# Performance work log

Measured on AMD Instinct MI355X. Metric: run time of the kernel, lower is better.

The kernel has to match this reference:

```python
import jax, jax.numpy as jnp
import numpy as np

R = 10000   # relation_num
E = 256     # emb_size == hidden_size
B = 1024    # batch
L = 8       # body length (loop runs L-1 steps)


def setup_inputs() -> dict:
    key = jax.random.key(0)
    ks = jax.random.split(key, 10)
    s = 0.05
    return {
        "bodys": jax.random.randint(ks[0], (B, L), 0, R),
        "emb_w": jax.random.normal(ks[1], (R, E), jnp.float32) * s,
        "w_ih": jax.random.normal(ks[2], (4 * E, E), jnp.float32) * s,
        "w_hh": jax.random.normal(ks[3], (4 * E, E), jnp.float32) * s,
        "b_ih": jax.random.normal(ks[4], (4 * E,), jnp.float32) * s,
        "b_hh": jax.random.normal(ks[5], (4 * E,), jnp.float32) * s,
        "fc1_w": jax.random.normal(ks[6], (E, 2 * E), jnp.float32) * s,
        "fc1_b": jax.random.normal(ks[7], (E,), jnp.float32) * s,
        "fc2_w": jax.random.normal(ks[8], (R + 1, E), jnp.float32) * s,
        "fc2_b": jax.random.normal(ks[9], (R + 1,), jnp.float32) * s,
    }


def _lstm(x, w_ih, w_hh, b_ih, b_hh):
    # x: [B, L, E] -> hidden states [B, L, H] (torch gate order i,f,g,o)
    Bn, _, H = x.shape[0], x.shape[1], w_hh.shape[1]
    h0 = jnp.zeros((Bn, H), x.dtype)
    c0 = jnp.zeros((Bn, H), x.dtype)

    def step(carry, xt):
        h, c = carry
        g = xt @ w_ih.T + b_ih + h @ w_hh.T + b_hh
        i, f, gg, o = jnp.split(g, 4, axis=-1)
        c = jax.nn.sigmoid(f) * c + jax.nn.sigmoid(i) * jnp.tanh(gg)
        h = jax.nn.sigmoid(o) * jnp.tanh(c)
        return (h, c), h

    _, hs = jax.lax.scan(step, (h0, c0), x.transpose(1, 0, 2))
    return hs.transpose(1, 0, 2)


def reference(bodys, emb_w, w_ih, w_hh, b_ih, b_hh, fc1_w, fc1_b, fc2_w, fc2_b):
    x = emb_w[bodys]                       # [B, L, E] embedded body relations
    body_hid = _lstm(x, w_ih, w_hh, b_ih, b_hh)  # [B, L, E]
    Rn = emb_w.shape[0]
    prob = emb_concat = prob_sf = None
    for i in range(body_hid.shape[1] - 1):   # short fixed unroll (L-1 steps)
        if i == 0:
            emb_1 = x[:, 0, :]
            second = x[:, 1, :]
        else:
            # prob_sf @ cat(embedding(indices), body_hid[:, i])  without [B,R+1,E]
            emb_1 = prob_sf[:, :Rn] @ emb_w + prob_sf[:, Rn:] * body_hid[:, i, :]
            # relation_emb[:, i+1, :] == emb_w[i+1] broadcast over batch
            second = jnp.broadcast_to(emb_w[i + 1], emb_1.shape)
        emb_concat = jnp.concatenate([emb_1, second], axis=1)   # [B, 2E]
        prob = jax.nn.relu(emb_concat @ fc1_w.T + fc1_b) @ fc2_w.T + fc2_b  # [B, R+1]
        prob_sf = jax.nn.softmax(prob, axis=1)
    return prob, emb_concat
```

## Files before the change

### kernel.cpp

```cpp
#include <hip/hip_runtime.h>

#define Bv 1024
#define Ev 256
#define Lv 8
#define Rv 10000
#define NP1 10001
#define PS2 10240
#define NPAD 10112
#define BM 64
#define BN 128
#define NSLICE 16
#define NSLOT 158
#define RPSTRIDE 160

typedef __attribute__((ext_vector_type(8))) short bf16x8;
typedef __attribute__((ext_vector_type(4))) float f32x4;

__device__ __forceinline__ float b2f(unsigned short u) {
    union { unsigned int i; float f; } v; v.i = ((unsigned int)u) << 16; return v.f;
}
__device__ __forceinline__ unsigned short f2b(float f) {
    union { float f; unsigned int i; } v; v.f = f;
    unsigned int r = v.i + 0x7fffu + ((v.i >> 16) & 1u);
    return (unsigned short)(r >> 16);
}
__device__ __forceinline__ void glds16(const void* g, void* l) {
    __builtin_amdgcn_global_load_lds(
        (const __attribute__((address_space(1))) void*)g,
        (__attribute__((address_space(3))) void*)l, 16, 0, 0);
}

__global__ __launch_bounds__(256) void gemm_tile(
    const unsigned short* __restrict__ A1, int lda1,
    const unsigned short* __restrict__ W1, int ldw1,
    const float* __restrict__ bias1,
    int Ktot, int kchunk, int Ncols, int mode,
    float* __restrict__ outF, unsigned short* __restrict__ outB, int ldc,
    float* __restrict__ rowPart, float* __restrict__ sfLastU)
{
    __shared__ unsigned short As[2][BM * 32];
    __shared__ unsigned short Bs[2][BN * 32];

    int bmode = mode & 7;
    int swz   = mode >> 4;
    int bx, by, bz;
    if (swz == 1) {
        int r = blockIdx.x & 7, q = blockIdx.x >> 3;
        bx = q & 15; by = r + (q >> 4) * 8; bz = 0;
        if (by >= NPAD / BN) return;
    } else if (swz == 2) {
        int r = blockIdx.x & 7, q = blockIdx.x >> 3;
        bz = r + (q >> 5) * 8; bx = (q & 31) >> 1; by = q & 1;
    } else {
        bx = blockIdx.x; by = blockIdx.y; bz = blockIdx.z;
    }

    int tid  = threadIdx.x;
    int wave = tid >> 6;
    int lane = tid & 63;
    int quad = lane >> 4;
    int l16  = lane & 15;
    int wm = (wave & 1) * 32;
    int wn = (wave >> 1) * 64;
    int m0 = bx * BM;
    int n0 = by * BN;
    int k0 = bz * kchunk;
    int k1 = k0 + kchunk; if (k1 > Ktot) k1 = Ktot;

    f32x4 acc[2][4];
#pragma unroll
    for (int i = 0; i < 2; ++i)
#pragma unroll
        for (int j = 0; j < 4; ++j) acc[i][j] = (f32x4){0.f, 0.f, 0.f, 0.f};

    int c0 = tid, c1 = 256 + tid;
    int row0 = c0 >> 2, row1 = c1 >> 2;
    int g80 = ((c0 & 3) ^ (row0 & 3) ^ ((row0 >> 2) & 3)) * 8;
    int g81 = ((c1 & 3) ^ (row1 & 3) ^ ((row1 >> 2) & 3)) * 8;

    bool first = true;
    for (int k = k0; k < k1; k += 64) {
        if (!first) __syncthreads();
        first = false;
#pragma unroll
        for (int h = 0; h < 2; ++h) {
            int kk = k + h * 32;
            glds16(A1 + (size_t)(m0 + row0) * lda1 + kk + g80, As[h] + (wave * 64) * 8);
            glds16(W1 + (size_t)(n0 + row0) * ldw1 + kk + g80, Bs[h] + (wave * 64) * 8);
            glds16(W1 + (size_t)(n0 + row1) * ldw1 + kk + g81, Bs[h] + (256 + wave * 64) * 8);
        }
        asm volatile("s_waitcnt vmcnt(0)" ::: "memory");
        __syncthreads();

#pragma unroll
        for (int h = 0; h < 2; ++h) {
            bf16x8 af[2], bfr[4];
#pragma unroll
            for (int t = 0; t < 2; ++t) {
                int m = wm + t * 16 + l16;
                int ca = quad ^ (m & 3) ^ ((m >> 2) & 3);
                af[t] = *(const bf16x8*)(As[h] + m * 32 + ca * 8);
            }
#pragma unroll
            for (int t = 0; t < 4; ++t) {
                int n = wn + t * 16 + l16;
                int cb = quad ^ (n & 3) ^ ((n >> 2) & 3);
                bfr[t] = *(const bf16x8*)(Bs[h] + n * 32 + cb * 8);
            }
#pragma unroll
            for (int i = 0; i < 2; ++i)
#pragma unroll
                for (int j = 0; j < 4; ++j)
                    acc[i][j] = __builtin_amdgcn_mfma_f32_16x16x32_bf16(
                        af[i], bfr[j], acc[i][j], 0, 0, 0);
        }
    }

    if (bmode == 5) {
        float rsum[2][4];
#pragma unroll
        for (int i = 0; i < 2; ++i)
#pragma unroll
            for (int r = 0; r < 4; ++r) rsum[i][r] = 0.f;
#pragma unroll
        for (int j = 0; j < 4; ++j) {
            int n = n0 + wn + j * 16 + l16;
            bool valid = (n < Ncols);
            float bsum = valid ? bias1[n] : 0.f;
#pragma unroll
            for (int i = 0; i < 2; ++i) {
                int mBase = m0 + wm + i * 16 + quad * 4;
#pragma unroll
                for (int r = 0; r < 4; ++r) {
                    float e = 0.f;
                    unsigned short w = 0;
                    if (valid) {
                        e = expf(acc[i][j][r] + bsum);
                        w = f2b(e);
                        if (n == Rv) sfLastU[mBase + r] = e;
                    }
                    outB[(size_t)(mBase + r) * ldc + n] = w;
                    rsum[i][r] += e;
                }
            }
        }
        int slot = by * 2 + (wn >> 6);
#pragma unroll
        for (int i = 0; i < 2; ++i)
#pragma unroll
            for (int r = 0; r < 4; ++r) {
                float s = rsum[i][r];
                s += __shfl_xor(s, 1);
                s += __shfl_xor(s, 2);
                s += __shfl_xor(s, 4);
                s += __shfl_xor(s, 8);
                if (l16 == 0) {
                    int m = m0 + wm + i * 16 + quad * 4 + r;
                    rowPart[(size_t)m * RPSTRIDE + slot] = s;
                }
            }
        return;
    }

#pragma unroll
    for (int j = 0; j < 4; ++j) {
        int n = n0 + wn + j * 16 + l16;
        bool valid = (n < Ncols);
        if (!valid && bmode != 3) continue;
        float bsum = (valid && bias1) ? bias1[n] : 0.f;
#pragma unroll
        for (int i = 0; i < 2; ++i) {
            int mBase = m0 + wm + i * 16 + quad * 4;
#pragma unroll
            for (int r = 0; r < 4; ++r) {
                float v = acc[i][j][r] + bsum;
                size_t idx = (size_t)(mBase + r) * ldc + n;
                if (bmode == 0)      outF[idx] = v;
                else if (bmode == 3) outB[idx] = valid ? f2b(v) : (unsigned short)0;
                else                 outB[(size_t)bz * (Bv * Ev) + idx] = f2b(v);
            }
        }
    }
}

__global__ __launch_bounds__(256) void gemm64(
    const unsigned short* __restrict__ A1, int lda1,
    const unsigned short* __restrict__ W1, int ldw1,
    const float* __restrict__ bias1,
    int Ktot, int Ncols, int mode,
    float* __restrict__ outF, unsigned short* __restrict__ outB,
    int ldc, int nshift,
    const float* __restrict__ xgate, int tstep)
{
    __shared__ unsigned short As[2][64 * 32];
    __shared__ unsigned short Bs[2][64 * 32];

    int bmode = mode & 7;
    int bx = blockIdx.x >> nshift;
    int by = blockIdx.x & ((1 << nshift) - 1);
    int tid  = threadIdx.x;
    int wave = tid >> 6;
    int lane = tid & 63;
    int quad = lane >> 4;
    int l16  = lane & 15;
    int m0 = bx * 64;
    int n0 = by * 64;

    f32x4 acc[4];
#pragma unroll
    for (int j = 0; j < 4; ++j) acc[j] = (f32x4){0.f, 0.f, 0.f, 0.f};

    int row = tid >> 2;
    int g8  = ((tid & 3) ^ (row & 3) ^ ((row >> 2) & 3)) * 8;

    bool first = true;
    for (int k = 0; k < Ktot; k += 64) {
        if (!first) __syncthreads();
        first = false;
#pragma unroll
        for (int h = 0; h < 2; ++h) {
            int kk = k + h * 32;
            glds16(A1 + (size_t)(m0 + row) * lda1 + kk + g8, As[h] + wave * 512);
            glds16(W1 + (size_t)(n0 + row) * ldw1 + kk + g8, Bs[h] + wave * 512);
        }
        asm volatile("s_waitcnt vmcnt(0)" ::: "memory");
        __syncthreads();

#pragma unroll
        for (int h = 0; h < 2; ++h) {
            int ml = wave * 16 + l16;
            int ca = quad ^ (ml & 3) ^ ((ml >> 2) & 3);
            bf16x8 a = *(const bf16x8*)(As[h] + ml * 32 + ca * 8);
#pragma unroll
            for (int j = 0; j < 4; ++j) {
                int nl = j * 16 + l16;
                int cb = quad ^ (nl & 3) ^ ((nl >> 2) & 3);
                bf16x8 b = *(const bf16x8*)(Bs[h] + nl * 32 + cb * 8);
                acc[j] = __builtin_amdgcn_mfma_f32_16x16x32_bf16(a, b, acc[j], 0, 0, 0);
            }
        }
    }

    if (bmode == 4) {
        int e  = by * 16 + l16;
        float bi = bias1[n0 + l16];
        float bf_ = bias1[n0 + 16 + l16];
        float bg = bias1[n0 + 32 + l16];
        float bo = bias1[n0 + 48 + l16];
#pragma unroll
        for (int r = 0; r < 4; ++r) {
            int m = m0 + wave * 16 + quad * 4 + r;
            const float* xr = xgate + ((size_t)m * Lv + tstep) * 1024 + n0 + l16;
            float gi = acc[0][r] + bi + xr[0];
            float gf = acc[1][r] + bf_ + xr[16];
            float gg = acc[2][r] + bg + xr[32];
            float go = acc[3][r] + bo + xr[48];
            float cp = (mode & 8) ? 0.f : outF[(size_t)m * 256 + e];
            float si = 1.f / (1.f + expf(-gi));
            float sf = 1.f / (1.f + expf(-gf));
            float so = 1.f / (1.f + expf(-go));
            float cn = sf * cp + si * tanhf(gg);
            outF[(size_t)m * 256 + e] = cn;
            outB[(size_t)m * 256 + e] = f2b(so * tanhf(cn));
        }
        return;
    }

#pragma unroll
    for (int j = 0; j < 4; ++j) {
        int n = n0 + j * 16 + l16;
        if (n >= Ncols) continue;
        float bsum = bias1 ? bias1[n] : 0.f;
#pragma unroll
        for (int r = 0; r < 4; ++r) {
            int m = m0 + wave * 16 + quad * 4 + r;
            float v = acc[j][r] + bsum;
            if (bmode == 1) outB[(size_t)m * ldc + n] = f2b(v > 0.f ? v : 0.f);
            else            outB[(size_t)m * ldc + n] = f2b(v);
        }
    }
}

__global__ void prep_k(const float* __restrict__ w_ih,
                       const float* __restrict__ w_hh,
                       const float* __restrict__ fc1_w,
                       const float* __restrict__ fc2_w,
                       const float* __restrict__ b_ih,
                       const float* __restrict__ b_hh,
                       const int* __restrict__ bodys,
                       const float* __restrict__ emb_w,
                       const float* __restrict__ fc1_b,
                       unsigned short* __restrict__ w_ih_b,
                       unsigned short* __restrict__ w_hh_b,
                       unsigned short* __restrict__ fc1_w_b,
                       unsigned short* __restrict__ fc2_w_b,
                       float* __restrict__ biasC,
                       unsigned short* __restrict__ x,
                       unsigned short* __restrict__ embT,
                       unsigned short* __restrict__ embc,
                       unsigned short* __restrict__ sfA,
                       float* __restrict__ B2,
                       unsigned short* __restrict__ emb_w_b,
                       unsigned short* __restrict__ EW1T)
{
    __shared__ float tile[32][33];
    int b = blockIdx.x, t = threadIdx.x;
    if (b < 1264) {
#pragma unroll
        for (int j = 0; j < 8; ++j) {
            int i = b * 2048 + j * 256 + t;
            fc2_w_b[i] = (i < NP1 * Ev) ? f2b(fc2_w[i]) : (unsigned short)0;
        }
    } else if (b < 1520) {
        int bb = b - 1264;
        const float* src = (bb < 128) ? w_ih : w_hh;
        unsigned short* dst = (bb < 128) ? w_ih_b : w_hh_b;
        int rb = (bb & 127) * 8;
#pragma unroll
        for (int j = 0; j < 8; ++j) {
            int r = rb + j;
            int gate = (r >> 4) & 3;
            int e = (r & 15) | ((r >> 6) << 4);
            dst[(size_t)r * 256 + t] = f2b(src[(size_t)(gate * 256 + e) * 256 + t]);
        }
    } else if (b < 1584) {
        int base = (b - 1520) * 2048;
#pragma unroll
        for (int j = 0; j < 8; ++j) {
            int i = base + j * 256 + t;
            fc1_w_b[i] = f2b(fc1_w[i]);
        }
    } else if (b < 1585) {
#pragma unroll
        for (int j = 0; j < 4; ++j) {
            int r = j * 256 + t;
            int gate = (r >> 4) & 3;
            int e = (r & 15) | ((r >> 6) << 4);
            biasC[r] = b_ih[gate * 256 + e] + b_hh[gate * 256 + e];
        }
    } else if (b < 2609) {
        int bb = b - 1585;
#pragma unroll
        for (int j = 0; j < 8; ++j) {
            int row = bb * 8 + j;
            x[(size_t)row * Ev + t] = f2b(emb_w[(size_t)bodys[row] * Ev + t]);
        }
    } else if (b < 5169) {
        int bb = b - 2609;
        int kt = (bb % 320) * 32, et = (bb / 320) * 32;
        int tx = t & 31, ty = t >> 5;
#pragma unroll
        for (int r = ty; r < 32; r += 8) {
            int k = kt + r;
            tile[r][tx] = (k < Rv) ? emb_w[(size_t)k * Ev + et + tx] : 0.f;
        }
        __syncthreads();
#pragma unroll
        for (int r = ty; r < 32; r += 8) {
            embT[(size_t)(et + r) * PS2 + kt + tx] = f2b(tile[tx][r]);
        }
    } else if (b < 6193) {
        int bb = b - 5169;
        embc[(size_t)bb * 512 + t]       = f2b(emb_w[(size_t)bodys[bb * Lv + 0] * Ev + t]);
        embc[(size_t)bb * 512 + 256 + t] = f2b(emb_w[(size_t)bodys[bb * Lv + 1] * Ev + t]);
        if (t < PS2 - NPAD) sfA[(size_t)bb * PS2 + NPAD + t] = 0;
    } else if (b < 6200) {
        int i = b - 6193;
        const float* er = emb_w + (size_t)(i + 1) * Ev;
        const float* wr = fc1_w + (size_t)t * 512 + 256;
        float s = fc1_b[t];
        for (int k = 0; k < 256; ++k) s += wr[k] * er[k];
        B2[i * 256 + t] = s;
    } else if (b < 7464) {
        int bb = b - 6200;
#pragma unroll
        for (int j = 0; j < 8; ++j) {
            int i = bb * 2048 + j * 256 + t;
            emb_w_b[i] = ((i >> 8) < Rv) ? f2b(emb_w[i]) : (unsigned short)0;
        }
    } else {
        int idx = (b - 7464) * 256 + t;
        EW1T[(size_t)(idx >> 7) * PS2 + NPAD + (idx & 127)] = 0;
    }
}

__global__ void finalize_emb(const unsigned short* __restrict__ emb1p,
                             const float* __restrict__ rowPart,
                             const float* __restrict__ sfLastU,
                             const unsigned short* __restrict__ h_i,
                             const float* __restrict__ emb_row,
                             unsigned short* __restrict__ embc,
                             float* __restrict__ outTail,
                             const float* __restrict__ HWrow,
                             const float* __restrict__ B2row,
                             unsigned short* __restrict__ hiddenA)
{
    int b = blockIdx.x, e = threadIdx.x;
    int wave = e >> 6, lane = e & 63;
    __shared__ float sred[4];
    float ps = (e < NSLOT) ? rowPart[(size_t)b * RPSTRIDE + e] : 0.f;
    for (int off = 32; off; off >>= 1) ps += __shfl_down(ps, off);
    if (lane == 0) sred[wave] = ps;
    __syncthreads();
    float inv = 1.f / (sred[0] + sred[1] + sred[2] + sred[3]);

    float x1 = 0.f;
#pragma unroll
    for (int z = 0; z < NSLICE; ++z)
        x1 += b2f(emb1p[(size_t)z * (Bv * Ev) + (size_t)b * Ev + e]);

    if (HWrow) {
        float v = x1 * inv + sfLastU[b] * inv * HWrow[(size_t)b * 256 + e] + B2row[e];
        hiddenA[(size_t)b * 256 + e] = f2b(v > 0.f ? v : 0.f);
    } else {
        float v = (x1 + sfLastU[b] * b2f(h_i[(size_t)b * Ev + e])) * inv;
        embc[(size_t)b * 512 + e] = f2b(v);
        float w = emb_row[e];
        embc[(size_t)b * 512 + 256 + e]    = f2b(w);
        outTail[(size_t)b * 512 + e]       = v;
        outTail[(size_t)b * 512 + 256 + e] = w;
    }
}

extern "C" void kernel_launch(void* const* d_in, const int* in_sizes, int n_in,
                              void* d_out, int out_size, void* d_ws, size_t ws_size,
                              hipStream_t stream)
{
    const int*   bodys = (const int*)d_in[0];
    const float* emb_w = (const float*)d_in[1];
    const float* w_ih  = (const float*)d_in[2];
    const float* w_hh  = (const float*)d_in[3];
    const float* b_ih  = (const float*)d_in[4];
    const float* b_hh  = (const float*)d_in[5];
    const float* fc1_w = (const float*)d_in[6];
    const float* fc1_b = (const float*)d_in[7];
    const float* fc2_w = (const float*)d_in[8];
    const float* fc2_b = (const float*)d_in[9];
    float* out = (float*)d_out;

    char* ws = (char*)d_ws;
    size_t off = 0;
    auto alloc = [&](size_t bytes) -> void* {
        void* p = ws + off;
        off += (bytes + 255) & ~(size_t)255;
        return p;
    };
    unsigned short* x       = (unsigned short*)alloc((size_t)Bv * Lv * Ev * 2);
    unsigned short* hs      = (unsigned short*)alloc((size_t)Lv * Bv * Ev * 2);
    float*          cbuf    = (float*)alloc((size_t)Bv * Ev * 4);
    float*          xg      = (float*)alloc((size_t)Bv * Lv * 1024 * 4);
    unsigned short* embT    = (unsigned short*)alloc((size_t)Ev * PS2 * 2);
    unsigned short* sfA     = (unsigned short*)alloc((size_t)Bv * PS2 * 2);
    float*          sfLastU = (float*)alloc((size_t)Bv * 4);
    float*          rowPart = (float*)alloc((size_t)Bv * RPSTRIDE * 4);
    unsigned short* emb1p   = (unsigned short*)alloc((size_t)NSLICE * Bv * Ev * 2);
    unsigned short* embc    = (unsigned short*)alloc((size_t)Bv * 512 * 2);
    unsigned short* hiddenA = (unsigned short*)alloc((size_t)Bv * Ev * 2);
    unsigned short* w_ih_b  = (unsigned short*)alloc((size_t)1024 * Ev * 2);
    unsigned short* w_hh_b  = (unsigned short*)alloc((size_t)1024 * Ev * 2);
    float*          biasC   = (float*)alloc((size_t)1024 * 4);
    float*          B2      = (float*)alloc((size_t)7 * 256 * 4);
    unsigned short* fc1_w_b = (unsigned short*)alloc((size_t)Ev * 512 * 2);
    unsigned short* fc2_w_b = (unsigned short*)alloc((size_t)NPAD * Ev * 2);
    unsigned short* emb_w_b = (unsigned short*)alloc((size_t)NPAD * Ev * 2);
    unsigned short* EW1T    = (unsigned short*)alloc((size_t)Ev * PS2 * 2);
    float*          HW      = (float*)alloc((size_t)Lv * Bv * Ev * 4);
    (void)ws_size; (void)in_sizes; (void)n_in; (void)out_size;

    prep_k<<<7592, 256, 0, stream>>>(w_ih, w_hh, fc1_w, fc2_w, b_ih, b_hh,
                                     bodys, emb_w, fc1_b,
                                     w_ih_b, w_hh_b, fc1_w_b, fc2_w_b, biasC, x,
                                     embT, embc, sfA, B2, emb_w_b, EW1T);

    gemm_tile<<<dim3(4, 79, 1), 256, 0, stream>>>(
        fc1_w_b, 512, emb_w_b, Ev,
        nullptr,
        Ev, Ev, Rv, 3,
        nullptr, EW1T, PS2, nullptr, nullptr);

    gemm64<<<64, 256, 0, stream>>>(
        embc, 512, fc1_w_b, 512,
        fc1_b,
        512, 256, 1,
        nullptr, hiddenA, 256, 2,
        nullptr, 0);

    gemm_tile<<<dim3(128, 8, 1), 256, 0, stream>>>(
        x, Ev, w_ih_b, Ev,
        nullptr,
        Ev, Ev, 1024, 0,
        xg, nullptr, 1024, nullptr, nullptr);

    for (int t = 0; t < Lv; ++t) {
        gemm64<<<256, 256, 0, stream>>>(
            hs + (size_t)(t ? t - 1 : 0) * Bv * Ev, Ev, w_hh_b, Ev,
            biasC,
            (t == 0) ? 0 : Ev, 1024, 4 | (t == 0 ? 8 : 0),
            cbuf, hs + (size_t)t * Bv * Ev, 1024, 4,
            xg, t);
    }

    gemm_tile<<<dim3(128, 2, 1), 256, 0, stream>>>(
        hs, Ev, fc1_w_b, 512,
        nullptr,
        Ev, Ev, Ev, 0,
        HW, nullptr, Ev, nullptr, nullptr);

    for (int i = 0; i < 7; ++i) {
        if (i > 0) {
            bool last = (i == 6);
            gemm_tile<<<512, 256, 0, stream>>>(
                sfA, PS2, last ? embT : EW1T, PS2,
                nullptr,
                PS2, PS2 / NSLICE, Ev, 2 | (2 << 4),
                nullptr, emb1p, Ev, nullptr, nullptr);
            finalize_emb<<<Bv, 256, 0, stream>>>(
                emb1p, rowPart, sfLastU,
                hs + (size_t)i * Bv * Ev, emb_w + (size_t)(i + 1) * Ev,
                embc, out + (size_t)Bv * NP1,
                last ? nullptr : (HW + (size_t)i * Bv * Ev),
                last ? nullptr : (B2 + (size_t)i * 256),
                hiddenA);
            if (last) {
                gemm64<<<64, 256, 0, stream>>>(
                    embc, 512, fc1_w_b, 512,
                    B2 + (size_t)6 * 256,
                    256, 256, 1,
                    nullptr, hiddenA, 256, 2,
                    nullptr, 0);
            }
        }
        if (i < 6) {
            gemm_tile<<<1280, 256, 0, stream>>>(
                hiddenA, Ev, fc2_w_b, Ev,
                fc2_b,
                Ev, Ev, NP1, 5 | (1 << 4),
                nullptr, sfA, PS2, rowPart, sfLastU);
        } else {
            gemm_tile<<<1280, 256, 0, stream>>>(
                hiddenA, Ev, fc2_w_b, Ev,
                fc2_b,
                Ev, Ev, NP1, 0 | (1 << 4),
                out, nullptr, NP1, nullptr, nullptr);
        }
    }
}
```

Baseline: 452.7 us.

## Fuse softmax-probability GEMM into fc2 epilogue with atomic accumulation

Adds a mode-6 epilogue to the fc2 GEMM. It keeps the exponentiated probability tile in LDS and immediately multiplies it by the matching EW1T slice, then atomically adds the partial results into an fp32 X1 buffer. This removes writing the [B, 10240] bf16 probability matrix to global memory and the separate split-K GEMM plus 16-slice reduction for the middle steps. In exchange it relies on many fp32 atomics and extra LDS, and it changes the ordering of floating-point accumulation. Shared memory is switched to dynamic allocation so the larger mode-6 footprint fits.

```diff
diff --git a/kernel.cpp b/kernel.cpp
--- a/kernel.cpp
+++ b/kernel.cpp
@@ -36,10 +36,14 @@
     const float* __restrict__ bias1,
     int Ktot, int kchunk, int Ncols, int mode,
     float* __restrict__ outF, unsigned short* __restrict__ outB, int ldc,
-    float* __restrict__ rowPart, float* __restrict__ sfLastU)
+    float* __restrict__ rowPart, float* __restrict__ sfLastU,
+    const unsigned short* __restrict__ PVB)
 {
-    __shared__ unsigned short As[2][BM * 32];
-    __shared__ unsigned short Bs[2][BN * 32];
+    extern __shared__ unsigned short smem[];
+    unsigned short* As0 = smem;
+    unsigned short* As1 = smem + 2048;
+    unsigned short* Bs0 = smem + 4096;
+    unsigned short* Bs1 = smem + 8192;
 
     int bmode = mode & 7;
     int swz   = mode >> 4;
@@ -85,27 +89,31 @@
 #pragma unroll
         for (int h = 0; h < 2; ++h) {
             int kk = k + h * 32;
-            glds16(A1 + (size_t)(m0 + row0) * lda1 + kk + g80, As[h] + (wave * 64) * 8);
-            glds16(W1 + (size_t)(n0 + row0) * ldw1 + kk + g80, Bs[h] + (wave * 64) * 8);
-            glds16(W1 + (size_t)(n0 + row1) * ldw1 + kk + g81, Bs[h] + (256 + wave * 64) * 8);
+            unsigned short* Ash = h ? As1 : As0;
+            unsigned short* Bsh = h ? Bs1 : Bs0;
+            glds16(A1 + (size_t)(m0 + row0) * lda1 + kk + g80, Ash + (wave * 64) * 8);
+            glds16(W1 + (size_t)(n0 + row0) * ldw1 + kk + g80, Bsh + (wave * 64) * 8);
+            glds16(W1 + (size_t)(n0 + row1) * ldw1 + kk + g81, Bsh + (256 + wave * 64) * 8);
         }
         asm volatile("s_waitcnt vmcnt(0)" ::: "memory");
         __syncthreads();
 
 #pragma unroll
         for (int h = 0; h < 2; ++h) {
+            const unsigned short* Ash = h ? As1 : As0;
+            const unsigned short* Bsh = h ? Bs1 : Bs0;
             bf16x8 af[2], bfr[4];
 #pragma unroll
             for (int t = 0; t < 2; ++t) {
                 int m = wm + t * 16 + l16;
                 int ca = quad ^ (m & 3) ^ ((m >> 2) & 3);
-                af[t] = *(const bf16x8*)(As[h] + m * 32 + ca * 8);
+                af[t] = *(const bf16x8*)(Ash + m * 32 + ca * 8);
             }
 #pragma unroll
             for (int t = 0; t < 4; ++t) {
                 int n = wn + t * 16 + l16;
                 int cb = quad ^ (n & 3) ^ ((n >> 2) & 3);
-                bfr[t] = *(const bf16x8*)(Bs[h] + n * 32 + cb * 8);
+                bfr[t] = *(const bf16x8*)(Bsh + n * 32 + cb * 8);
             }
 #pragma unroll
             for (int i = 0; i < 2; ++i)
@@ -116,20 +124,25 @@
         }
     }
 
-    if (bmode == 5) {
+    if (bmode == 5 || bmode == 6) {
         float rsum[2][4];
 #pragma unroll
         for (int i = 0; i < 2; ++i)
 #pragma unroll
             for (int r = 0; r < 4; ++r) rsum[i][r] = 0.f;
+
+        if (bmode == 6) __syncthreads();
+        unsigned short* Ps = smem;
+
 #pragma unroll
         for (int j = 0; j < 4; ++j) {
-            int n = n0 + wn + j * 16 + l16;
+            int nl = wn + j * 16 + l16;
+            int n  = n0 + nl;
             bool valid = (n < Ncols);
             float bsum = valid ? bias1[n] : 0.f;
 #pragma unroll
             for (int i = 0; i < 2; ++i) {
-                int mBase = m0 + wm + i * 16 + quad * 4;
+                int mlB = wm + i * 16 + quad * 4;
 #pragma unroll
                 for (int r = 0; r < 4; ++r) {
                     float e = 0.f;
@@ -137,9 +150,14 @@
                     if (valid) {
                         e = expf(acc[i][j][r] + bsum);
                         w = f2b(e);
-                        if (n == Rv) sfLastU[mBase + r] = e;
+                        if (n == Rv) sfLastU[m0 + mlB + r] = e;
                     }
-                    outB[(size_t)(mBase + r) * ldc + n] = w;
+                    if (bmode == 5) {
+                        outB[(size_t)(m0 + mlB + r) * ldc + n] = w;
+                    } else {
+                        int ml = mlB + r;
+                        Ps[ml * 128 + ((((nl >> 3) ^ (ml & 7)) << 3) | (nl & 7))] = w;
+                    }
                     rsum[i][r] += e;
                 }
             }
@@ -157,6 +175,59 @@
                 if (l16 == 0) {
                     int m = m0 + wm + i * 16 + quad * 4 + r;
                     rowPart[(size_t)m * RPSTRIDE + slot] = s;
+                }
+            }
+        if (bmode == 5) return;
+
+        unsigned short* Bst = smem + 8192;
+        f32x4 pv[4][4];
+#pragma unroll
+        for (int mi = 0; mi < 4; ++mi)
+#pragma unroll
+            for (int ej = 0; ej < 4; ++ej) pv[mi][ej] = (f32x4){0.f, 0.f, 0.f, 0.f};
+
+        for (int ks = 0; ks < 4; ++ks) {
+            __syncthreads();
+#pragma unroll
+            for (int cc = 0; cc < 4; ++cc) {
+                int c = cc * 256 + tid;
+                int row = c >> 2;
+                int g = ((c & 3) ^ (row & 3) ^ ((row >> 2) & 3)) * 8;
+                glds16(PVB + (size_t)row * PS2 + n0 + ks * 32 + g,
+                       Bst + (size_t)(cc * 256 + wave * 64) * 8);
+            }
+            asm volatile("s_waitcnt vmcnt(0)" ::: "memory");
+            __syncthreads();
+
+            bf16x8 pa[4], eb[4];
+#pragma unroll
+            for (int mi = 0; mi < 4; ++mi) {
+                int ml = mi * 16 + l16;
+                int oct = ks * 4 + quad;
+                pa[mi] = *(const bf16x8*)(Ps + ml * 128 + ((oct ^ (ml & 7)) << 3));
+            }
+#pragma unroll
+            for (int ej = 0; ej < 4; ++ej) {
+                int e = wave * 64 + ej * 16 + l16;
+                int cb = quad ^ (e & 3) ^ ((e >> 2) & 3);
+                eb[ej] = *(const bf16x8*)(Bst + e * 32 + cb * 8);
+            }
+#pragma unroll
+            for (int mi = 0; mi < 4; ++mi)
+#pragma unroll
+                for (int ej = 0; ej < 4; ++ej)
+                    pv[mi][ej] = __builtin_amdgcn_mfma_f32_16x16x32_bf16(
+                        pa[mi], eb[ej], pv[mi][ej], 0, 0, 0);
+        }
+#pragma unroll
+        for (int mi = 0; mi < 4; ++mi)
+#pragma unroll
+            for (int ej = 0; ej < 4; ++ej) {
+                int e = wave * 64 + ej * 16 + l16;
+#pragma unroll
+                for (int r = 0; r < 4; ++r) {
+                    int m = m0 + mi * 16 + quad * 4 + r;
+                    atomicAdd(&outF[(size_t)m * 256 + e], pv[mi][ej][r]);
                 }
             }
         return;
@@ -301,7 +372,8 @@
                        unsigned short* __restrict__ sfA,
                        float* __restrict__ B2,
                        unsigned short* __restrict__ emb_w_b,
-                       unsigned short* __restrict__ EW1T)
+                       unsigned short* __restrict__ EW1T,
+                       float* __restrict__ X1)
 {
     __shared__ float tile[32][33];
     int b = blockIdx.x, t = threadIdx.x;
@@ -364,6 +436,7 @@
         embc[(size_t)bb * 512 + t]       = f2b(emb_w[(size_t)bodys[bb * Lv + 0] * Ev + t]);
         embc[(size_t)bb * 512 + 256 + t] = f2b(emb_w[(size_t)bodys[bb * Lv + 1] * Ev + t]);
         if (t < PS2 - NPAD) sfA[(size_t)bb * PS2 + NPAD + t] = 0;
+        X1[(size_t)bb * 256 + t] = 0.f;
     } else if (b < 6200) {
         int i = b - 6193;
         const float* er = emb_w + (size_t)(i + 1) * Ev;
@@ -385,6 +458,7 @@
 }
 
 __global__ void finalize_emb(const unsigned short* __restrict__ emb1p,
+                             float* __restrict__ X1f,
                              const float* __restrict__ rowPart,
                              const float* __restrict__ sfLastU,
                              const unsigned short* __restrict__ h_i,
@@ -404,15 +478,16 @@
     __syncthreads();
     float inv = 1.f / (sred[0] + sred[1] + sred[2] + sred[3]);
 
-    float x1 = 0.f;
-#pragma unroll
-    for (int z = 0; z < NSLICE; ++z)
-        x1 += b2f(emb1p[(size_t)z * (Bv * Ev) + (size_t)b * Ev + e]);
-
-    if (HWrow) {
-        float v = x1 * inv + sfLastU[b] * inv * HWrow[(size_t)b * 256 + e] + B2row[e];
-        hiddenA[(size_t)b * 256 + e] = f2b(v > 0.f ? v : 0.f);
+    if (X1f) {
+        size_t idx = (size_t)b * 256 + e;
+        float v = X1f[idx] * inv + sfLastU[b] * inv * HWrow[idx] + B2row[e];
+        hiddenA[idx] = f2b(v > 0.f ? v : 0.f);
+        X1f[idx] = 0.f;
     } else {
+        float x1 = 0.f;
+#pragma unroll
+        for (int z = 0; z < NSLICE; ++z)
+            x1 += b2f(emb1p[(size_t)z * (Bv * Ev) + (size_t)b * Ev + e]);
         float v = (x1 + sfLastU[b] * b2f(h_i[(size_t)b * Ev + e])) * inv;
         embc[(size_t)b * 512 + e] = f2b(v);
         float w = emb_row[e];
@@ -465,18 +540,19 @@
     unsigned short* emb_w_b = (unsigned short*)alloc((size_t)NPAD * Ev * 2);
     unsigned short* EW1T    = (unsigned short*)alloc((size_t)Ev * PS2 * 2);
     float*          HW      = (float*)alloc((size_t)Lv * Bv * Ev * 4);
+    float*          X1      = (float*)alloc((size_t)Bv * Ev * 4);
     (void)ws_size; (void)in_sizes; (void)n_in; (void)out_size;
 
     prep_k<<<7592, 256, 0, stream>>>(w_ih, w_hh, fc1_w, fc2_w, b_ih, b_hh,
                                      bodys, emb_w, fc1_b,
                                      w_ih_b, w_hh_b, fc1_w_b, fc2_w_b, biasC, x,
-                                     embT, embc, sfA, B2, emb_w_b, EW1T);
-
-    gemm_tile<<<dim3(4, 79, 1), 256, 0, stream>>>(
+                                     embT, embc, sfA, B2, emb_w_b, EW1T, X1);
+
+    gemm_tile<<<dim3(4, 79, 1), 256, 24576, stream>>>(
         fc1_w_b, 512, emb_w_b, Ev,
         nullptr,
         Ev, Ev, Rv, 3,
-        nullptr, EW1T, PS2, nullptr, nullptr);
+        nullptr, EW1T, PS2, nullptr, nullptr, nullptr);
 
     gemm64<<<64, 256, 0, stream>>>(
         embc, 512, fc1_w_b, 512,
@@ -485,11 +561,11 @@
         nullptr, hiddenA, 256, 2,
         nullptr, 0);
 
-    gemm_tile<<<dim3(128, 8, 1), 256, 0, stream>>>(
+    gemm_tile<<<dim3(128, 8, 1), 256, 24576, stream>>>(
         x, Ev, w_ih_b, Ev,
         nullptr,
         Ev, Ev, 1024, 0,
-        xg, nullptr, 1024, nullptr, nullptr);
+        xg, nullptr, 1024, nullptr, nullptr, nullptr);
 
     for (int t = 0; t < Lv; ++t) {
         gemm64<<<256, 256, 0, stream>>>(
@@ -500,48 +576,55 @@
             xg, t);
     }
 
-    gemm_tile<<<dim3(128, 2, 1), 256, 0, stream>>>(
+    gemm_tile<<<dim3(128, 2, 1), 256, 24576, stream>>>(
         hs, Ev, fc1_w_b, 512,
         nullptr,
         Ev, Ev, Ev, 0,
-        HW, nullptr, Ev, nullptr, nullptr);
+        HW, nullptr, Ev, nullptr, nullptr, nullptr);
 
     for (int i = 0; i < 7; ++i) {
-        if (i > 0) {
-            bool last = (i == 6);
-            gemm_tile<<<512, 256, 0, stream>>>(
-                sfA, PS2, last ? embT : EW1T, PS2,
+        if (i > 0 && i < 6) {
+            finalize_emb<<<Bv, 256, 0, stream>>>(
+                nullptr, X1, rowPart, sfLastU,
+                nullptr, nullptr, nullptr, nullptr,
+                HW + (size_t)i * Bv * Ev, B2 + (size_t)i * 256,
+                hiddenA);
+        } else if (i == 6) {
+            gemm_tile<<<512, 256, 24576, stream>>>(
+                sfA, PS2, embT, PS2,
                 nullptr,
                 PS2, PS2 / NSLICE, Ev, 2 | (2 << 4),
-                nullptr, emb1p, Ev, nullptr, nullptr);
+                nullptr, emb1p, Ev, nullptr, nullptr, nullptr);
             finalize_emb<<<Bv, 256, 0, stream>>>(
-                emb1p, rowPart, sfLastU,
-                hs + (size_t)i * Bv * Ev, emb_w + (size_t)(i + 1) * Ev,
+                emb1p, nullptr, rowPart, sfLastU,
+                hs + (size_t)6 * Bv * Ev, emb_w + (size_t)7 * Ev,
                 embc, out + (size_t)Bv * NP1,
-                last ? nullptr : (HW + (size_t)i * Bv * Ev),
-                last ? nullptr : (B2 + (size_t)i * 256),
-                hiddenA);
-            if (last) {
-                gemm64<<<64, 256, 0, stream>>>(
-                    embc, 512, fc1_w_b, 512,
-                    B2 + (size_t)6 * 256,
-                    256, 256, 1,
-                    nullptr, hiddenA, 256, 2,
-                    nullptr, 0);
-            }
-        }
-        if (i < 6) {
-            gemm_tile<<<1280, 256, 0, stream>>>(
+                nullptr, nullptr, hiddenA);
+            gemm64<<<64, 256, 0, stream>>>(
+                embc, 512, fc1_w_b, 512,
+                B2 + (size_t)6 * 256,
+                256, 256, 1,
+                nullptr, hiddenA, 256, 2,
+                nullptr, 0);
+        }
+        if (i < 5) {
+            gemm_tile<<<1280, 256, 32768, stream>>>(
+                hiddenA, Ev, fc2_w_b, Ev,
+                fc2_b,
+                Ev, Ev, NP1, 6 | (1 << 4),
+                X1, nullptr, PS2, rowPart, sfLastU, EW1T);
+        } else if (i == 5) {
+            gemm_tile<<<1280, 256, 24576, stream>>>(
                 hiddenA, Ev, fc2_w_b, Ev,
                 fc2_b,
                 Ev, Ev, NP1, 5 | (1 << 4),
-                nullptr, sfA, PS2, rowPart, sfLastU);
+                nullptr, sfA, PS2, rowPart, sfLastU, nullptr);
         } else {
-            gemm_tile<<<1280, 256, 0, stream>>>(
+            gemm_tile<<<1280, 256, 24576, stream>>>(
                 hiddenA, Ev, fc2_w_b, Ev,
                 fc2_b,
                 Ev, Ev, NP1, 0 | (1 << 4),
-                out, nullptr, NP1, nullptr, nullptr);
-        }
-    }
-}
+                out, nullptr, NP1, nullptr, nullptr, nullptr);
+        }
+    }
+}
```

After: 682.4 us. 50.8% more time.
